# Kernel optimization log

Hardware: AMD Instinct MI355X
Metric: run time of the kernel (lower is better)

The kernel has to match this reference:

```python
import jax, jax.numpy as jnp
import numpy as np

D, M, R, N = 64, 256, 3, 1024
L_MID = 2  # number of middle phi layers (L=4 total)


def sp10(x):
    # torch.nn.Softplus(beta=10)
    return jax.nn.softplus(10.0 * x) / 10.0


def setup_inputs() -> dict:
    key = jax.random.key(0)
    ks = jax.random.split(key, 16)
    w_scale = 1.0 / np.sqrt(R)
    a_ht_scale = 0.1 / np.sqrt(M)
    inp = {
        "X": jax.random.uniform(ks[0], (N, D), dtype=jnp.float32),
        "w_first": 1.0 * jax.random.normal(ks[1], (D, M, 1, R), dtype=jnp.float32),
        "w_mid": w_scale * jax.random.normal(ks[2], (L_MID, D, M, R, R), dtype=jnp.float32),
        "w_last": w_scale * jax.random.normal(ks[3], (D, M, R, 1), dtype=jnp.float32),
        "b_first": 0.1 * jax.random.normal(ks[4], (D, M, R), dtype=jnp.float32),
        "b_mid": 0.1 * jax.random.normal(ks[5], (L_MID, D, M, R), dtype=jnp.float32),
        "b_last": 0.1 * jax.random.normal(ks[6], (D, M, 1), dtype=jnp.float32),
        "a_first": jax.random.normal(ks[7], (D, M, R), dtype=jnp.float32),
        "a_mid": jax.random.normal(ks[8], (L_MID, D, M, R), dtype=jnp.float32),
    }
    # HT mixing matrices: init m*eye(m) per group (as in source) + small noise
    dims = [32, 16, 8, 4, 2]
    for i, g in enumerate(dims):
        eye = M * jnp.eye(M, dtype=jnp.float32)
        inp[f"aHT{i}"] = jnp.tile(eye[None], (g, 1, 1)) + 0.01 * jax.random.normal(ks[9 + i], (g, M, M), dtype=jnp.float32)
    inp["aHT5"] = a_ht_scale * jax.random.normal(ks[15], (1, M, 1), dtype=jnp.float32)
    return inp


def _layer(phis, phidots, w, b, a):
    # one hidden layer of the per-(d,m) rank-r MLP chain
    W = sp10(w)                                            # (d,m,k,l) >= 0
    z = jnp.einsum('ndmk,dmkl->ndml', phis, W) + b         # affine
    tz = jnp.tanh(z)
    ta = jnp.tanh(a)
    phidots = jnp.einsum('ndmk,dmkl->ndml', phidots, W) * (1.0 + ta * (1.0 - tz * tz))
    phis = z + tz * ta
    return phis, phidots


def _forward(X, w_first, w_mid, w_last, b_first, b_mid, b_last, a_first, a_mid,
             aHT0, aHT1, aHT2, aHT3, aHT4, aHT5):
    n = X.shape[0]
    phis = jnp.broadcast_to(X[:, :, None, None], (n, D, M, 1))  # expand_X
    phidots = jnp.ones_like(phis)
    phis, phidots = _layer(phis, phidots, w_first, b_first, a_first)
    for i in range(w_mid.shape[0]):
        phis, phidots = _layer(phis, phidots, w_mid[i], b_mid[i], a_mid[i])
    Wl = sp10(w_last)
    z = jnp.einsum('ndmk,dmkl->ndml', phis, Wl) + b_last   # (n,d,m,1)
    s = jax.nn.sigmoid(z)
    phidots = (jnp.einsum('ndmk,dmkl->ndml', phidots, Wl) * (s * (1.0 - s)))[..., 0]  # (n,d,m)
    # HT contraction: default couplings = consecutive pairs, d=64 -> 6 levels
    T = phidots
    for a in (aHT0, aHT1, aHT2, aHT3, aHT4, aHT5):
        nn_, dim, m_ = T.shape
        T = T.reshape(nn_, dim // 2, 2, m_).prod(axis=2)   # product over each pair
        A = sp10(a)
        A = A / A.sum(axis=1, keepdims=True)               # column-normalized nonneg mix
        T = jnp.einsum('ngm,gmk->ngk', T, A)
    return T[:, 0, 0]                                      # likelihood, shape (n,)


def reference(X, w_first, w_mid, w_last, b_first, b_mid, b_last, a_first, a_mid,
              aHT0, aHT1, aHT2, aHT3, aHT4, aHT5):
    return _forward(X, w_first, w_mid, w_last, b_first, b_mid, b_last,
                    a_first, a_mid, aHT0, aHT1, aHT2, aHT3, aHT4, aHT5)
```

## Files before the change

kernel.cpp:

```cpp
#include <hip/hip_runtime.h>
#include <cstdint>
#include <cstddef>

#define D_DIM 64
#define M_DIM 256
#define N_PTS 1024

typedef __attribute__((ext_vector_type(4))) float f32x4;
typedef __attribute__((ext_vector_type(2))) float f32x2;
typedef __attribute__((ext_vector_type(8))) short s16x8;
typedef unsigned int u32;

static __device__ __forceinline__ void cp16(const unsigned short* g,
                                            unsigned short* l) {
    const __attribute__((address_space(1))) u32* gp =
        (const __attribute__((address_space(1))) u32*)g;
    __attribute__((address_space(3))) u32* lp =
        (__attribute__((address_space(3))) u32*)l;
    __builtin_amdgcn_global_load_lds(gp, lp, 16, 0, 0);
}

static __device__ __forceinline__ f32x2 pkfma(f32x2 a, f32x2 b, f32x2 c) {
#if __has_builtin(__builtin_elementwise_fma)
    return __builtin_elementwise_fma(a, b, c);
#else
    f32x2 r; r.x = fmaf(a.x, b.x, c.x); r.y = fmaf(a.y, b.y, c.y); return r;
#endif
}
static __device__ __forceinline__ f32x2 sp2(float s) {
    f32x2 r; r.x = s; r.y = s; return r;
}

static __device__ __forceinline__ float sp10f(float x) {
    float t = 10.f * x;
    return 0.1f * (fmaxf(t, 0.f) + log1pf(__expf(-fabsf(t))));
}

static __device__ __forceinline__ f32x2 ftanh2(f32x2 x) {
    f32x2 xs = x * sp2(2.88539008177793f);
    f32x2 e;
    e.x = __builtin_amdgcn_exp2f(xs.x);
    e.y = __builtin_amdgcn_exp2f(xs.y);
    f32x2 ep = e + sp2(1.f);
    f32x2 r;
    r.x = __builtin_amdgcn_rcpf(ep.x);
    r.y = __builtin_amdgcn_rcpf(ep.y);
    return pkfma(sp2(-2.f), r, sp2(1.f));
}

static __device__ __forceinline__ unsigned short f2bf(float x) {
    unsigned u = __float_as_uint(x);
    u = u + 0x7FFFu + ((u >> 16) & 1u);
    return (unsigned short)(u >> 16);
}
static __device__ __forceinline__ float bf2f(unsigned short h) {
    return __uint_as_float(((unsigned)h) << 16);
}

static __device__ __forceinline__ void split1(float x, unsigned& uh, unsigned& ul) {
    unsigned u = __float_as_uint(x);
    uh = u + 0x7FFFu + ((u >> 16) & 1u);
    ul = __float_as_uint(x - __uint_as_float(uh & 0xFFFF0000u));
}

static __device__ __forceinline__ const float* map_g(int g, const float* a0, const float* a1,
                                                     const float* a2, const float* a3,
                                                     const float* a4, int& lg) {
    if (g < 32) { lg = g;      return a0; }
    if (g < 48) { lg = g - 32; return a1; }
    if (g < 56) { lg = g - 48; return a2; }
    if (g < 60) { lg = g - 56; return a3; }
    lg = g - 60; return a4;
}

__global__ __launch_bounds__(256) void k_prep3(
    const float* __restrict__ X, const float* __restrict__ wf,
    const float* __restrict__ wm, const float* __restrict__ wl,
    const float* __restrict__ b1, const float* __restrict__ bm,
    const float* __restrict__ bl, const float* __restrict__ af,
    const float* __restrict__ am,
    const float* __restrict__ a0, const float* __restrict__ a1,
    const float* __restrict__ a2, const float* __restrict__ a3,
    const float* __restrict__ a4,
    float* __restrict__ Wpack, float* __restrict__ Xt,
    unsigned short* __restrict__ Anth, unsigned short* __restrict__ Antl) {
    __shared__ float tile[64][65];
    const int t = threadIdx.x;
    const int b = blockIdx.x;
    if (b < 16) {
        const int n0 = b * 64;
#pragma unroll
        for (int i = 0; i < 4; i++) {
            const int f   = i * 256 + t;
            const int row = f >> 4;
            const int c4  = f & 15;
            float4 v = *(const float4*)(X + (size_t)(n0 + row) * 64 + c4 * 4);
            tile[row][c4 * 4 + 0] = v.x;
            tile[row][c4 * 4 + 1] = v.y;
            tile[row][c4 * 4 + 2] = v.z;
            tile[row][c4 * 4 + 3] = v.w;
        }
        __syncthreads();
#pragma unroll
        for (int i = 0; i < 4; i++) {
            const int f    = i * 256 + t;
            const int drow = f >> 4;
            const int c4   = f & 15;
            float4 v;
            v.x = tile[c4 * 4 + 0][drow];
            v.y = tile[c4 * 4 + 1][drow];
            v.z = tile[c4 * 4 + 2][drow];
            v.w = tile[c4 * 4 + 3][drow];
            *(float4*)(Xt + (size_t)drow * 1024 + n0 + c4 * 4) = v;
        }
        return;
    }
    if (b < 80) {
        const int id = (b - 16) * 256 + t;
        float r[48];
#pragma unroll
        for (int q = 0; q < 48; q++) r[q] = 0.f;
#pragma unroll
        for (int q = 0; q < 3; q++) {
            r[0 + q] = sp10f(wf[id * 3 + q]);
            r[3 + q] = b1[id * 3 + q];
            r[6 + q] = tanhf(af[id * 3 + q]);
            r[39 + q] = sp10f(wl[id * 3 + q]);
        }
#pragma unroll
        for (int l = 0; l < 2; l++) {
            const size_t b9 = ((size_t)l * 16384 + id) * 9;
            const size_t b3 = ((size_t)l * 16384 + id) * 3;
#pragma unroll
            for (int q = 0; q < 9; q++) r[9 + l * 15 + q] = sp10f(wm[b9 + q]);
#pragma unroll
            for (int q = 0; q < 3; q++) {
                r[18 + l * 15 + q] = bm[b3 + q];
                r[21 + l * 15 + q] = tanhf(am[b3 + q]);
            }
        }
        r[42] = bl[id];
        float4* o = (float4*)(Wpack + (size_t)id * 48);
#pragma unroll
        for (int q = 0; q < 12; q++) o[q] = ((float4*)r)[q];
        return;
    }
    const int idx = b - 80;
    const int g   = idx >> 4;
    const int rr  = idx & 15;
    const int m0  = (rr & 3) * 64;
    const int k0  = (rr >> 2) * 64;
    int lg;
    const float* A  = map_g(g, a0, a1, a2, a3, a4, lg);
    const float* Ag = A + (size_t)lg * 65536;

#pragma unroll
    for (int i = 0; i < 4; i++) {
        const int f   = i * 256 + t;
        const int row = f >> 4;
        const int c4  = f & 15;
        float4 v = *(const float4*)(Ag + (size_t)(m0 + row) * 256 + k0 + c4 * 4);
        tile[row][c4 * 4 + 0] = v.x;
        tile[row][c4 * 4 + 1] = v.y;
        tile[row][c4 * 4 + 2] = v.z;
        tile[row][c4 * 4 + 3] = v.w;
    }
    __syncthreads();

#pragma unroll
    for (int i = 0; i < 4; i++) {
        const int f    = i * 256 + t;
        const int krow = f >> 4;
        const int c4   = f & 15;
        float v0 = sp10f(tile[c4 * 4 + 0][krow]);
        float v1 = sp10f(tile[c4 * 4 + 1][krow]);
        float v2 = sp10f(tile[c4 * 4 + 2][krow]);
        float v3 = sp10f(tile[c4 * 4 + 3][krow]);
        unsigned short h0 = f2bf(v0), h1 = f2bf(v1), h2 = f2bf(v2), h3 = f2bf(v3);
        ushort4 hi, lo;
        hi.x = h0; hi.y = h1; hi.z = h2; hi.w = h3;
        lo.x = f2bf(v0 - bf2f(h0));
        lo.y = f2bf(v1 - bf2f(h1));
        lo.z = f2bf(v2 - bf2f(h2));
        lo.w = f2bf(v3 - bf2f(h3));
        const size_t dst = (size_t)g * 65536 + (size_t)(k0 + krow) * 256 + m0 + c4 * 4;
        *(ushort4*)(Anth + dst) = hi;
        *(ushort4*)(Antl + dst) = lo;
    }
}

__global__ void k_csum_t(const unsigned short* __restrict__ Anth,
                         const unsigned short* __restrict__ Antl,
                         float* __restrict__ csum) {
    const int g    = blockIdx.x;
    const int w    = threadIdx.x >> 6;
    const int lane = threadIdx.x & 63;
    const int k    = blockIdx.y * 4 + w;
    const size_t base = (size_t)g * 65536 + k * 256 + lane * 4;
    uint2 vh = *(const uint2*)(Anth + base);
    uint2 vl = *(const uint2*)(Antl + base);
    float s = 0.f;
    s += bf2f((unsigned short)(vh.x & 0xFFFFu)) + bf2f((unsigned short)(vh.x >> 16));
    s += bf2f((unsigned short)(vh.y & 0xFFFFu)) + bf2f((unsigned short)(vh.y >> 16));
    s += bf2f((unsigned short)(vl.x & 0xFFFFu)) + bf2f((unsigned short)(vl.x >> 16));
    s += bf2f((unsigned short)(vl.y & 0xFFFFu)) + bf2f((unsigned short)(vl.y >> 16));
    for (int off = 32; off > 0; off >>= 1) s += __shfl_down(s, off);
    if (lane == 0) csum[g * 256 + k] = s;
}

__global__ __launch_bounds__(512, 1) void k_phase1(
    const float* __restrict__ Xt, const float* __restrict__ Wpack,
    unsigned short* __restrict__ P0h, unsigned short* __restrict__ P0l) {
    __shared__ float sT[128][33];
    __shared__ float sXd[2][128];
    const int j  = blockIdx.x;
    const int mc = blockIdx.y;
    const int n0 = blockIdx.z * 128;
    const int t  = threadIdx.x;
    const int w    = __builtin_amdgcn_readfirstlane(t >> 6);
    const int lane = t & 63;

    if (t < 256)
        sXd[t >> 7][t & 127] = Xt[(size_t)(2 * j + (t >> 7)) * 1024 + n0 + (t & 127)];
    __syncthreads();

    f32x2 xe0, xe1;
    xe0.x = sXd[0][lane]; xe0.y = sXd[0][64 + lane];
    xe1.x = sXd[1][lane]; xe1.y = sXd[1][64 + lane];

    const f32x2 one2 = sp2(1.f);
    f32x2 p0;

#pragma unroll 2
    for (int it = 0; it < 8; it++) {
        const int i  = it >> 1;
        const int e  = it & 1;
        const int mm = w * 4 + i;
        const int m  = mc * 32 + mm;
        const float* __restrict__ rp =
            Wpack + (size_t)(((2 * j + e) << 8) + m) * 48;
        float W1a[3], B1a[3], T1a[3], Wm[2][9], Bm[2][3], Tm[2][3], Wla[3];
#pragma unroll
        for (int r = 0; r < 3; r++) {
            W1a[r] = rp[r];
            B1a[r] = rp[3 + r];
            T1a[r] = rp[6 + r];
            Bm[0][r] = rp[18 + r];
            Tm[0][r] = rp[21 + r];
            Bm[1][r] = rp[33 + r];
            Tm[1][r] = rp[36 + r];
            Wla[r] = rp[39 + r];
        }
#pragma unroll
        for (int q = 0; q < 9; q++) {
            Wm[0][q] = rp[9 + q];
            Wm[1][q] = rp[24 + q];
        }
        const float Bla = rp[42];

        const f32x2 x = e ? xe1 : xe0;
        f32x2 phi[3], pd[3];
#pragma unroll
        for (int r = 0; r < 3; r++) {
            f32x2 z  = pkfma(x, sp2(W1a[r]), sp2(B1a[r]));
            f32x2 tz = ftanh2(z);
            f32x2 ta = sp2(T1a[r]);
            pd[r]  = sp2(W1a[r]) * pkfma(ta, pkfma(-tz, tz, one2), one2);
            phi[r] = pkfma(tz, ta, z);
        }
#pragma unroll
        for (int l = 0; l < 2; l++) {
            f32x2 nphi[3], npd[3];
#pragma unroll
            for (int q = 0; q < 3; q++) {
                f32x2 z  = sp2(Bm[l][q]);
                f32x2 dp = sp2(0.f);
#pragma unroll
                for (int r = 0; r < 3; r++) {
                    f32x2 wv = sp2(Wm[l][r * 3 + q]);
                    z  = pkfma(phi[r], wv, z);
                    dp = pkfma(pd[r],  wv, dp);
                }
                f32x2 tz = ftanh2(z);
                f32x2 ta = sp2(Tm[l][q]);
                nphi[q] = pkfma(tz, ta, z);
                npd[q]  = dp * pkfma(ta, pkfma(-tz, tz, one2), one2);
            }
#pragma unroll
            for (int q = 0; q < 3; q++) { phi[q] = nphi[q]; pd[q] = npd[q]; }
        }
        f32x2 z  = sp2(Bla);
        f32x2 dp = sp2(0.f);
#pragma unroll
        for (int r = 0; r < 3; r++) {
            f32x2 wv = sp2(Wla[r]);
            z  = pkfma(phi[r], wv, z);
            dp = pkfma(pd[r],  wv, dp);
        }
        f32x2 zs = z * sp2(-1.4426950408889634f);
        f32x2 s;
        s.x = __builtin_amdgcn_rcpf(1.f + __builtin_amdgcn_exp2f(zs.x));
        s.y = __builtin_amdgcn_rcpf(1.f + __builtin_amdgcn_exp2f(zs.y));
        f32x2 prod = dp * s * (one2 - s);
        if (e == 0) {
            p0 = prod;
        } else {
            sT[lane][mm]      = p0.x * prod.x;
            sT[64 + lane][mm] = p0.y * prod.y;
        }
    }
    __syncthreads();

    const size_t base = ((size_t)j * N_PTS + n0) * M_DIM + mc * 32;
#pragma unroll
    for (int it = 0; it < 2; it++) {
        const int idx = it * 512 + t;
        const int row = idx >> 3;
        const int c4  = idx & 7;
        float4 v;
        v.x = sT[row][c4 * 4 + 0];
        v.y = sT[row][c4 * 4 + 1];
        v.z = sT[row][c4 * 4 + 2];
        v.w = sT[row][c4 * 4 + 3];
        unsigned uh0, ul0, uh1, ul1, uh2, ul2, uh3, ul3;
        split1(v.x, uh0, ul0);
        split1(v.y, uh1, ul1);
        split1(v.z, uh2, ul2);
        split1(v.w, uh3, ul3);
        uint2 hp, lp;
        hp.x = __builtin_amdgcn_perm(uh1, uh0, 0x07060302u);
        hp.y = __builtin_amdgcn_perm(uh3, uh2, 0x07060302u);
        lp.x = __builtin_amdgcn_perm(ul1, ul0, 0x07060302u);
        lp.y = __builtin_amdgcn_perm(ul3, ul2, 0x07060302u);
        *(uint2*)(P0h + base + (size_t)row * M_DIM + c4 * 4) = hp;
        *(uint2*)(P0l + base + (size_t)row * M_DIM + c4 * 4) = lp;
    }
}

#define LDST64 72

__global__ __launch_bounds__(256, 4) void k_g64ps(
    const unsigned short* __restrict__ Th, const unsigned short* __restrict__ Tl,
    const unsigned short* __restrict__ Bh, const unsigned short* __restrict__ Bl,
    const float* __restrict__ csum, float* __restrict__ Tout) {
    __shared__ unsigned short sAh[64 * 64];
    __shared__ unsigned short sAl[64 * 64];
    __shared__ unsigned short sBh[64 * 64];
    __shared__ unsigned short sBl[64 * 64];

    const int g  = blockIdx.z;
    const int n0 = blockIdx.x * 64;
    const int k0 = blockIdx.y * 64;
    const unsigned short* Thg = Th + ((size_t)g << 18);
    const unsigned short* Tlg = Tl + ((size_t)g << 18);
    const unsigned short* Bhg = Bh + ((size_t)g << 16);
    const unsigned short* Blg = Bl + ((size_t)g << 16);

    const int tid  = threadIdx.x;
    const int lane = tid & 63;
    const int w    = tid >> 6;
    const int wr   = w >> 1;
    const int wc   = w & 1;
    const int lr   = lane & 15;
    const int lk   = lane >> 4;

    f32x4 acc[2][2];
#pragma unroll
    for (int a = 0; a < 2; a++)
#pragma unroll
        for (int b = 0; b < 2; b++) acc[a][b] = (f32x4){0.f, 0.f, 0.f, 0.f};

    for (int kb = 0; kb < 256; kb += 64) {
#pragma unroll
        for (int i = 0; i < 2; i++) {
            const int idx      = i * 256 + tid;
            const int idx_base = i * 256 + (w << 6);
            const int row  = idx >> 3;
            const int slot = idx & 7;
            const int cslot = slot ^ (row & 7);
            const size_t srcA = (size_t)(n0 + row) * 256 + kb + cslot * 8;
            const size_t srcB = (size_t)(k0 + row) * 256 + kb + cslot * 8;
            cp16(Thg + srcA, sAh + (size_t)idx_base * 8);
            cp16(Tlg + srcA, sAl + (size_t)idx_base * 8);
            cp16(Bhg + srcB, sBh + (size_t)idx_base * 8);
            cp16(Blg + srcB, sBl + (size_t)idx_base * 8);
        }
        __syncthreads();

        s16x8 ah[2][2], al[2][2], bh[2][2], bl[2][2];
#pragma unroll
        for (int nt = 0; nt < 2; nt++)
#pragma unroll
            for (int ks = 0; ks < 2; ks++) {
                const int row = wr * 32 + nt * 16 + lr;
                const int cs  = (ks * 4 + lk) ^ (row & 7);
                const int off = row * 64 + cs * 8;
                ah[nt][ks] = *(const s16x8*)&sAh[off];
                al[nt][ks] = *(const s16x8*)&sAl[off];
            }
#pragma unroll
        for (int kt = 0; kt < 2; kt++)
#pragma unroll
            for (int ks = 0; ks < 2; ks++) {
                const int row = wc * 32 + kt * 16 + lr;
                const int cs  = (ks * 4 + lk) ^ (row & 7);
                const int off = row * 64 + cs * 8;
                bh[kt][ks] = *(const s16x8*)&sBh[off];
                bl[kt][ks] = *(const s16x8*)&sBl[off];
            }
#pragma unroll
        for (int ks = 0; ks < 2; ks++)
#pragma unroll
            for (int nt = 0; nt < 2; nt++)
#pragma unroll
                for (int kt = 0; kt < 2; kt++) {
                    acc[nt][kt] = __builtin_amdgcn_mfma_f32_16x16x32_bf16(ah[nt][ks], bh[kt][ks], acc[nt][kt], 0, 0, 0);
                    acc[nt][kt] = __builtin_amdgcn_mfma_f32_16x16x32_bf16(ah[nt][ks], bl[kt][ks], acc[nt][kt], 0, 0, 0);
                    acc[nt][kt] = __builtin_amdgcn_mfma_f32_16x16x32_bf16(al[nt][ks], bh[kt][ks], acc[nt][kt], 0, 0, 0);
                }
        __syncthreads();
    }

    float* Og = Tout + ((size_t)g << 18);
#pragma unroll
    for (int kt = 0; kt < 2; kt++) {
        const int col = k0 + wc * 32 + kt * 16 + lr;
        const float inv = 1.0f / csum[g * 256 + col];
#pragma unroll
        for (int nt = 0; nt < 2; nt++) {
            const int rbase = n0 + wr * 32 + nt * 16 + lk * 4;
#pragma unroll
            for (int r = 0; r < 4; r++)
                Og[(size_t)(rbase + r) * 256 + col] = acc[nt][kt][r] * inv;
        }
    }
}

__global__ __launch_bounds__(256, 4) void k_gemm64(const float* __restrict__ Tin,
                                                   const unsigned short* __restrict__ Bh,
                                                   const unsigned short* __restrict__ Bl,
                                                   const float* __restrict__ csum,
                                                   float* __restrict__ Tout) {
    __shared__ unsigned short sAh[64 * LDST64];
    __shared__ unsigned short sAl[64 * LDST64];
    __shared__ unsigned short sBh[64 * 64];
    __shared__ unsigned short sBl[64 * 64];

    const int g  = blockIdx.z;
    const int n0 = blockIdx.x * 64;
    const int k0 = blockIdx.y * 64;
    const float* T0  = Tin + (size_t)(2 * g) * N_PTS * 256;
    const float* T1p = T0 + (size_t)N_PTS * 256;
    const unsigned short* Bhg = Bh + ((size_t)g << 16);
    const unsigned short* Blg = Bl + ((size_t)g << 16);

    const int tid  = threadIdx.x;
    const int lane = tid & 63;
    const int w    = tid >> 6;
    const int wr   = w >> 1;
    const int wc   = w & 1;
    const int lr   = lane & 15;
    const int lk   = lane >> 4;

    f32x4 acc[2][2];
#pragma unroll
    for (int a = 0; a < 2; a++)
#pragma unroll
        for (int b = 0; b < 2; b++) acc[a][b] = (f32x4){0.f, 0.f, 0.f, 0.f};

    for (int kb = 0; kb < 256; kb += 64) {
#pragma unroll
        for (int i = 0; i < 2; i++) {
            const int idx      = i * 256 + tid;
            const int idx_base = i * 256 + (w << 6);
            const int row  = idx >> 3;
            const int slot = idx & 7;
            const int cslot = slot ^ (row & 7);
            const size_t srcB = (size_t)(k0 + row) * 256 + kb + cslot * 8;
            cp16(Bhg + srcB, sBh + (size_t)idx_base * 8);
            cp16(Blg + srcB, sBl + (size_t)idx_base * 8);
        }
#pragma unroll
        for (int i = 0; i < 4; i++) {
            const int idx = i * 256 + tid;
            const int row = idx >> 4;
            const int c4  = idx & 15;
            float4 v = *(const float4*)(T0 + (size_t)(n0 + row) * 256 + kb + c4 * 4);
            float4 u = *(const float4*)(T1p + (size_t)(n0 + row) * 256 + kb + c4 * 4);
            v.x *= u.x; v.y *= u.y; v.z *= u.z; v.w *= u.w;
            const unsigned b0 = __float_as_uint(v.x);
            const unsigned b1 = __float_as_uint(v.y);
            const unsigned b2 = __float_as_uint(v.z);
            const unsigned b3 = __float_as_uint(v.w);
            uint2 hp, lp;
            hp.x = __builtin_amdgcn_perm(b1, b0, 0x07060302u);
            hp.y = __builtin_amdgcn_perm(b3, b2, 0x07060302u);
            const float l0 = v.x - __uint_as_float(b0 & 0xFFFF0000u);
            const float l1 = v.y - __uint_as_float(b1 & 0xFFFF0000u);
            const float l2 = v.z - __uint_as_float(b2 & 0xFFFF0000u);
            const float l3 = v.w - __uint_as_float(b3 & 0xFFFF0000u);
            lp.x = __builtin_amdgcn_perm(__float_as_uint(l1), __float_as_uint(l0), 0x07060302u);
            lp.y = __builtin_amdgcn_perm(__float_as_uint(l3), __float_as_uint(l2), 0x07060302u);
            *(uint2*)&sAh[row * LDST64 + c4 * 4] = hp;
            *(uint2*)&sAl[row * LDST64 + c4 * 4] = lp;
        }
        __syncthreads();

        s16x8 ah[2][2], al[2][2], bh[2][2], bl[2][2];
#pragma unroll
        for (int nt = 0; nt < 2; nt++)
#pragma unroll
            for (int ks = 0; ks < 2; ks++) {
                const int off = (wr * 32 + nt * 16 + lr) * LDST64 + ks * 32 + lk * 8;
                ah[nt][ks] = *(const s16x8*)&sAh[off];
                al[nt][ks] = *(const s16x8*)&sAl[off];
            }
#pragma unroll
        for (int kt = 0; kt < 2; kt++)
#pragma unroll
            for (int ks = 0; ks < 2; ks++) {
                const int row = wc * 32 + kt * 16 + lr;
                const int cs  = (ks * 4 + lk) ^ (row & 7);
                const int off = row * 64 + cs * 8;
                bh[kt][ks] = *(const s16x8*)&sBh[off];
                bl[kt][ks] = *(const s16x8*)&sBl[off];
            }
#pragma unroll
        for (int ks = 0; ks < 2; ks++)
#pragma unroll
            for (int nt = 0; nt < 2; nt++)
#pragma unroll
                for (int kt = 0; kt < 2; kt++) {
                    acc[nt][kt] = __builtin_amdgcn_mfma_f32_16x16x32_bf16(ah[nt][ks], bh[kt][ks], acc[nt][kt], 0, 0, 0);
                    acc[nt][kt] = __builtin_amdgcn_mfma_f32_16x16x32_bf16(ah[nt][ks], bl[kt][ks], acc[nt][kt], 0, 0, 0);
                    acc[nt][kt] = __builtin_amdgcn_mfma_f32_16x16x32_bf16(al[nt][ks], bh[kt][ks], acc[nt][kt], 0, 0, 0);
                }
        __syncthreads();
    }

    float* Og = Tout + ((size_t)g << 18);
#pragma unroll
    for (int kt = 0; kt < 2; kt++) {
        const int col = k0 + wc * 32 + kt * 16 + lr;
        const float inv = 1.0f / csum[g * 256 + col];
#pragma unroll
        for (int nt = 0; nt < 2; nt++) {
            const int rbase = n0 + wr * 32 + nt * 16 + lk * 4;
#pragma unroll
            for (int r = 0; r < 4; r++)
                Og[(size_t)(rbase + r) * 256 + col] = acc[nt][kt][r] * inv;
        }
    }
}

__global__ void k_l5(const float* __restrict__ Tin, const float* __restrict__ a5,
                     float* __restrict__ out) {
    const int n = blockIdx.x;
    const int m = threadIdx.x;
    __shared__ float sv[256], sw[256];
    float w = sp10f(a5[m]);
    float v = Tin[(size_t)n * 256 + m] * Tin[(size_t)(N_PTS + n) * 256 + m] * w;
    sv[m] = v;
    sw[m] = w;
    __syncthreads();
    for (int s = 128; s > 0; s >>= 1) {
        if (m < s) { sv[m] += sv[m + s]; sw[m] += sw[m + s]; }
        __syncthreads();
    }
    if (m == 0) out[n] = sv[0] / sw[0];
}

extern "C" void kernel_launch(void* const* d_in, const int* in_sizes, int n_in,
                              void* d_out, int out_size, void* d_ws, size_t ws_size,
                              hipStream_t stream) {
    const float* X  = (const float*)d_in[0];
    const float* wf = (const float*)d_in[1];
    const float* wm = (const float*)d_in[2];
    const float* wl = (const float*)d_in[3];
    const float* b1 = (const float*)d_in[4];
    const float* bm = (const float*)d_in[5];
    const float* bl = (const float*)d_in[6];
    const float* af = (const float*)d_in[7];
    const float* am = (const float*)d_in[8];
    const float* a0 = (const float*)d_in[9];
    const float* a1 = (const float*)d_in[10];
    const float* a2 = (const float*)d_in[11];
    const float* a3 = (const float*)d_in[12];
    const float* a4 = (const float*)d_in[13];
    const float* a5 = (const float*)d_in[14];
    float* out = (float*)d_out;

    float* ws    = (float*)d_ws;
    float* Wpack = ws;
    float* Xt    = Wpack + 786432;
    float* csum  = Xt + 65536;
    unsigned short* Anth = (unsigned short*)(csum + 15872);
    unsigned short* Antl = Anth + (size_t)62 * 65536;
    float* B0    = (float*)(Antl + (size_t)62 * 65536);
    float* B1    = B0 + (size_t)32 * N_PTS * M_DIM;
    unsigned short* P0h = (unsigned short*)B1;
    unsigned short* P0l = P0h + (size_t)32 * N_PTS * M_DIM;

    k_prep3<<<1072, 256, 0, stream>>>(X, wf, wm, wl, b1, bm, bl, af, am,
                                      a0, a1, a2, a3, a4, Wpack, Xt, Anth, Antl);
    k_csum_t<<<dim3(62, 64), 256, 0, stream>>>(Anth, Antl, csum);
    k_phase1<<<dim3(32, 8, 8), 512, 0, stream>>>(Xt, Wpack, P0h, P0l);

    k_g64ps<<<dim3(16, 4, 32), 256, 0, stream>>>(P0h, P0l, Anth, Antl, csum, B0);
    k_gemm64<<<dim3(16, 4, 16), 256, 0, stream>>>(B0, Anth + (size_t)32 * 65536,
                                                  Antl + (size_t)32 * 65536, csum + 32 * 256, B1);
    k_gemm64<<<dim3(16, 4, 8), 256, 0, stream>>>(B1, Anth + (size_t)48 * 65536,
                                                 Antl + (size_t)48 * 65536, csum + 48 * 256, B0);
    k_gemm64<<<dim3(16, 4, 4), 256, 0, stream>>>(B0, Anth + (size_t)56 * 65536,
                                                 Antl + (size_t)56 * 65536, csum + 56 * 256, B1);
    k_gemm64<<<dim3(16, 4, 2), 256, 0, stream>>>(B1, Anth + (size_t)60 * 65536,
                                                 Antl + (size_t)60 * 65536, csum + 60 * 256, B0);
    k_l5<<<N_PTS, 256, 0, stream>>>(B0, a5, out);
}
```

Measured before the change: 145.4 us.

## Move HT matrix transpose/split into phase1 kernel launch to shrink prep kernel

Measured after the change: 146.3 us. About the same (+0.6%).

```diff
diff --git a/kernel.cpp b/kernel.cpp
--- a/kernel.cpp
+++ b/kernel.cpp
@@ -73,17 +73,13 @@
     lg = g - 60; return a4;
 }
 
-__global__ __launch_bounds__(256) void k_prep3(
+__global__ __launch_bounds__(256) void k_prep_s(
     const float* __restrict__ X, const float* __restrict__ wf,
     const float* __restrict__ wm, const float* __restrict__ wl,
     const float* __restrict__ b1, const float* __restrict__ bm,
     const float* __restrict__ bl, const float* __restrict__ af,
     const float* __restrict__ am,
-    const float* __restrict__ a0, const float* __restrict__ a1,
-    const float* __restrict__ a2, const float* __restrict__ a3,
-    const float* __restrict__ a4,
-    float* __restrict__ Wpack, float* __restrict__ Xt,
-    unsigned short* __restrict__ Anth, unsigned short* __restrict__ Antl) {
+    float* __restrict__ Wpack, float* __restrict__ Xt) {
     __shared__ float tile[64][65];
     const int t = threadIdx.x;
     const int b = blockIdx.x;
@@ -115,78 +111,33 @@
         }
         return;
     }
-    if (b < 80) {
-        const int id = (b - 16) * 256 + t;
-        float r[48];
-#pragma unroll
-        for (int q = 0; q < 48; q++) r[q] = 0.f;
+    const int id = (b - 16) * 256 + t;
+    float r[48];
+#pragma unroll
+    for (int q = 0; q < 48; q++) r[q] = 0.f;
+#pragma unroll
+    for (int q = 0; q < 3; q++) {
+        r[0 + q] = sp10f(wf[id * 3 + q]);
+        r[3 + q] = b1[id * 3 + q];
+        r[6 + q] = tanhf(af[id * 3 + q]);
+        r[39 + q] = sp10f(wl[id * 3 + q]);
+    }
+#pragma unroll
+    for (int l = 0; l < 2; l++) {
+        const size_t b9 = ((size_t)l * 16384 + id) * 9;
+        const size_t b3 = ((size_t)l * 16384 + id) * 3;
+#pragma unroll
+        for (int q = 0; q < 9; q++) r[9 + l * 15 + q] = sp10f(wm[b9 + q]);
 #pragma unroll
         for (int q = 0; q < 3; q++) {
-            r[0 + q] = sp10f(wf[id * 3 + q]);
-            r[3 + q] = b1[id * 3 + q];
-            r[6 + q] = tanhf(af[id * 3 + q]);
-            r[39 + q] = sp10f(wl[id * 3 + q]);
-        }
-#pragma unroll
-        for (int l = 0; l < 2; l++) {
-            const size_t b9 = ((size_t)l * 16384 + id) * 9;
-            const size_t b3 = ((size_t)l * 16384 + id) * 3;
-#pragma unroll
-            for (int q = 0; q < 9; q++) r[9 + l * 15 + q] = sp10f(wm[b9 + q]);
-#pragma unroll
-            for (int q = 0; q < 3; q++) {
-                r[18 + l * 15 + q] = bm[b3 + q];
-                r[21 + l * 15 + q] = tanhf(am[b3 + q]);
-            }
-        }
-        r[42] = bl[id];
-        float4* o = (float4*)(Wpack + (size_t)id * 48);
-#pragma unroll
-        for (int q = 0; q < 12; q++) o[q] = ((float4*)r)[q];
-        return;
-    }
-    const int idx = b - 80;
-    const int g   = idx >> 4;
-    const int rr  = idx & 15;
-    const int m0  = (rr & 3) * 64;
-    const int k0  = (rr >> 2) * 64;
-    int lg;
-    const float* A  = map_g(g, a0, a1, a2, a3, a4, lg);
-    const float* Ag = A + (size_t)lg * 65536;
-
-#pragma unroll
-    for (int i = 0; i < 4; i++) {
-        const int f   = i * 256 + t;
-        const int row = f >> 4;
-        const int c4  = f & 15;
-        float4 v = *(const float4*)(Ag + (size_t)(m0 + row) * 256 + k0 + c4 * 4);
-        tile[row][c4 * 4 + 0] = v.x;
-        tile[row][c4 * 4 + 1] = v.y;
-        tile[row][c4 * 4 + 2] = v.z;
-        tile[row][c4 * 4 + 3] = v.w;
-    }
-    __syncthreads();
-
-#pragma unroll
-    for (int i = 0; i < 4; i++) {
-        const int f    = i * 256 + t;
-        const int krow = f >> 4;
-        const int c4   = f & 15;
-        float v0 = sp10f(tile[c4 * 4 + 0][krow]);
-        float v1 = sp10f(tile[c4 * 4 + 1][krow]);
-        float v2 = sp10f(tile[c4 * 4 + 2][krow]);
-        float v3 = sp10f(tile[c4 * 4 + 3][krow]);
-        unsigned short h0 = f2bf(v0), h1 = f2bf(v1), h2 = f2bf(v2), h3 = f2bf(v3);
-        ushort4 hi, lo;
-        hi.x = h0; hi.y = h1; hi.z = h2; hi.w = h3;
-        lo.x = f2bf(v0 - bf2f(h0));
-        lo.y = f2bf(v1 - bf2f(h1));
-        lo.z = f2bf(v2 - bf2f(h2));
-        lo.w = f2bf(v3 - bf2f(h3));
-        const size_t dst = (size_t)g * 65536 + (size_t)(k0 + krow) * 256 + m0 + c4 * 4;
-        *(ushort4*)(Anth + dst) = hi;
-        *(ushort4*)(Antl + dst) = lo;
-    }
+            r[18 + l * 15 + q] = bm[b3 + q];
+            r[21 + l * 15 + q] = tanhf(am[b3 + q]);
+        }
+    }
+    r[42] = bl[id];
+    float4* o = (float4*)(Wpack + (size_t)id * 48);
+#pragma unroll
+    for (int q = 0; q < 12; q++) o[q] = ((float4*)r)[q];
 }
 
 __global__ void k_csum_t(const unsigned short* __restrict__ Anth,
@@ -208,25 +159,80 @@
     if (lane == 0) csum[g * 256 + k] = s;
 }
 
-__global__ __launch_bounds__(512, 1) void k_phase1(
+__global__ __launch_bounds__(512, 1) void k_p1tr(
     const float* __restrict__ Xt, const float* __restrict__ Wpack,
-    unsigned short* __restrict__ P0h, unsigned short* __restrict__ P0l) {
-    __shared__ float sT[128][33];
-    __shared__ float sXd[2][128];
-    const int j  = blockIdx.x;
-    const int mc = blockIdx.y;
-    const int n0 = blockIdx.z * 128;
-    const int t  = threadIdx.x;
+    unsigned short* __restrict__ P0h, unsigned short* __restrict__ P0l,
+    const float* __restrict__ a0, const float* __restrict__ a1,
+    const float* __restrict__ a2, const float* __restrict__ a3,
+    const float* __restrict__ a4,
+    unsigned short* __restrict__ Anth, unsigned short* __restrict__ Antl) {
+    __shared__ float smem[128 * 33 + 256];
+    const int t = threadIdx.x;
+
+    if (blockIdx.x < 992) {
+        float (*tile)[65] = (float(*)[65])smem;
+        const int idx = blockIdx.x;
+        const int g   = idx >> 4;
+        const int rr  = idx & 15;
+        const int m0  = (rr & 3) * 64;
+        const int k0  = (rr >> 2) * 64;
+        int lg;
+        const float* A  = map_g(g, a0, a1, a2, a3, a4, lg);
+        const float* Ag = A + (size_t)lg * 65536;
+
+#pragma unroll
+        for (int i = 0; i < 2; i++) {
+            const int f   = i * 512 + t;
+            const int row = f >> 4;
+            const int c4  = f & 15;
+            float4 v = *(const float4*)(Ag + (size_t)(m0 + row) * 256 + k0 + c4 * 4);
+            tile[row][c4 * 4 + 0] = v.x;
+            tile[row][c4 * 4 + 1] = v.y;
+            tile[row][c4 * 4 + 2] = v.z;
+            tile[row][c4 * 4 + 3] = v.w;
+        }
+        __syncthreads();
+
+#pragma unroll
+        for (int i = 0; i < 2; i++) {
+            const int f    = i * 512 + t;
+            const int krow = f >> 4;
+            const int c4   = f & 15;
+            float v0 = sp10f(tile[c4 * 4 + 0][krow]);
+            float v1 = sp10f(tile[c4 * 4 + 1][krow]);
+            float v2 = sp10f(tile[c4 * 4 + 2][krow]);
+            float v3 = sp10f(tile[c4 * 4 + 3][krow]);
+            unsigned short h0 = f2bf(v0), h1 = f2bf(v1), h2 = f2bf(v2), h3 = f2bf(v3);
+            ushort4 hi, lo;
+            hi.x = h0; hi.y = h1; hi.z = h2; hi.w = h3;
+            lo.x = f2bf(v0 - bf2f(h0));
+            lo.y = f2bf(v1 - bf2f(h1));
+            lo.z = f2bf(v2 - bf2f(h2));
+            lo.w = f2bf(v3 - bf2f(h3));
+            const size_t dst = (size_t)g * 65536 + (size_t)(k0 + krow) * 256 + m0 + c4 * 4;
+            *(ushort4*)(Anth + dst) = hi;
+            *(ushort4*)(Antl + dst) = lo;
+        }
+        return;
+    }
+
+    float (*sT)[33] = (float(*)[33])smem;
+    float* sXd = smem + 128 * 33;
+    const int bid = blockIdx.x - 992;
+    const int j  = bid & 31;
+    const int mc = (bid >> 5) & 7;
+    const int n0 = (bid >> 8) * 128;
     const int w    = __builtin_amdgcn_readfirstlane(t >> 6);
     const int lane = t & 63;
 
     if (t < 256)
-        sXd[t >> 7][t & 127] = Xt[(size_t)(2 * j + (t >> 7)) * 1024 + n0 + (t & 127)];
+        sXd[(t >> 7) * 128 + (t & 127)] =
+            Xt[(size_t)(2 * j + (t >> 7)) * 1024 + n0 + (t & 127)];
     __syncthreads();
 
     f32x2 xe0, xe1;
-    xe0.x = sXd[0][lane]; xe0.y = sXd[0][64 + lane];
-    xe1.x = sXd[1][lane]; xe1.y = sXd[1][64 + lane];
+    xe0.x = sXd[lane];       xe0.y = sXd[64 + lane];
+    xe1.x = sXd[128 + lane]; xe1.y = sXd[192 + lane];
 
     const f32x2 one2 = sp2(1.f);
     f32x2 p0;
@@ -601,10 +607,10 @@
     unsigned short* P0h = (unsigned short*)B1;
     unsigned short* P0l = P0h + (size_t)32 * N_PTS * M_DIM;
 
-    k_prep3<<<1072, 256, 0, stream>>>(X, wf, wm, wl, b1, bm, bl, af, am,
-                                      a0, a1, a2, a3, a4, Wpack, Xt, Anth, Antl);
+    k_prep_s<<<80, 256, 0, stream>>>(X, wf, wm, wl, b1, bm, bl, af, am, Wpack, Xt);
+    k_p1tr<<<3040, 512, 0, stream>>>(Xt, Wpack, P0h, P0l,
+                                     a0, a1, a2, a3, a4, Anth, Antl);
     k_csum_t<<<dim3(62, 64), 256, 0, stream>>>(Anth, Antl, csum);
-    k_phase1<<<dim3(32, 8, 8), 512, 0, stream>>>(Xt, Wpack, P0h, P0l);
 
     k_g64ps<<<dim3(16, 4, 32), 256, 0, stream>>>(P0h, P0l, Anth, Antl, csum, B0);
     k_gemm64<<<dim3(16, 4, 16), 256, 0, stream>>>(B0, Anth + (size_t)32 * 65536,
```
